# Performance work log

Measured on AMD Instinct MI355X. Metric: run time of the kernel, lower is better.

## Reference

```python
import jax, jax.numpy as jnp
import numpy as np

MARGIN = 1.0
EPS = 1e-05
B = 8192
D = 128
NUM_CLASSES = 256


def setup_inputs() -> dict:
    key = jax.random.key(0)
    k1, k2 = jax.random.split(key)
    feature = jax.random.normal(k1, (B, D), dtype=jnp.float32)
    label = jax.random.randint(k2, (B,), 0, NUM_CLASSES, dtype=jnp.int32)
    return {"feature": feature, "label": label}


def reference(feature, label):
    # Pairwise Euclidean distance matrix: ||x_i||^2 + ||x_j||^2 - 2 x_i.x_j + eps, then sqrt
    sq = jnp.sum(feature * feature, axis=1, keepdims=True)  # [B, 1]
    dist = jnp.sqrt(jnp.maximum(sq + sq.T - 2.0 * (feature @ feature.T) + EPS, 0.0))  # [B, B]

    same = label[:, None] == label[None, :]  # [B, B] bool, includes self on diagonal
    inf = jnp.array(jnp.inf, dtype=dist.dtype)

    # Original sorts each row and takes same[1]: the SECOND smallest same-label distance
    # (the smallest is the anchor itself, distance sqrt(eps)).
    d_same = jnp.where(same, dist, inf)
    two_smallest = -jax.lax.top_k(-d_same, 2)[0]  # [B, 2], ascending smallest two
    pos = two_smallest[:, 1]  # nearest positive excluding self

    # diff.min(): hardest (closest) negative per row
    neg = jnp.min(jnp.where(same, inf, dist), axis=1)

    hinge = jnp.maximum(MARGIN + pos - neg, 0.0)
    return jnp.mean(hinge)
```

## Files before the change

kernel.cpp:

```cpp
#include <hip/hip_runtime.h>
#include <math.h>


#define BN 8192
#define MARGIN_F 1.0f
#define EPS_F 1e-5f

typedef __attribute__((ext_vector_type(8))) short short8;
typedef __attribute__((ext_vector_type(4))) float floatx4;

__device__ __forceinline__ unsigned short bf16_rne(float x, float& r) {
    unsigned u = __float_as_uint(x);
    u += 0x7FFF + ((u >> 16) & 1);
    unsigned short h = (unsigned short)(u >> 16);
    r = __uint_as_float(((unsigned)h) << 16);
    return h;
}

__global__ __launch_bounds__(256) void prep_kernel(const float* __restrict__ f,
                                                   const int* __restrict__ lbl,
                                                   short8* __restrict__ fbT,
                                                   float2* __restrict__ lsq,
                                                   float* __restrict__ g_acc,
                                                   unsigned* __restrict__ counter) {
    int gid = blockIdx.x * 256 + threadIdx.x;
    if (gid == 0) { *g_acc = 0.f; *counter = 0u; }
    int row = gid >> 3, part = gid & 7;
    const float4* f4 = (const float4*)f + (size_t)row * 32 + part * 4;
    float s = 0.f;
#pragma unroll
    for (int cc = 0; cc < 2; ++cc) {
        float4 v0 = f4[cc * 2], v1 = f4[cc * 2 + 1];
        float r0, r1, r2, r3, r4, r5, r6, r7;
        short8 o;
        o[0] = (short)bf16_rne(v0.x, r0);
        o[1] = (short)bf16_rne(v0.y, r1);
        o[2] = (short)bf16_rne(v0.z, r2);
        o[3] = (short)bf16_rne(v0.w, r3);
        o[4] = (short)bf16_rne(v1.x, r4);
        o[5] = (short)bf16_rne(v1.y, r5);
        o[6] = (short)bf16_rne(v1.z, r6);
        o[7] = (short)bf16_rne(v1.w, r7);
        fbT[(size_t)(part * 2 + cc) * BN + row] = o;
        s += r0 * r0 + r1 * r1 + r2 * r2 + r3 * r3 +
             r4 * r4 + r5 * r5 + r6 * r6 + r7 * r7;
    }
    s += __shfl_xor(s, 1, 8);
    s += __shfl_xor(s, 2, 8);
    s += __shfl_xor(s, 4, 8);
    if (part == 0) {
        float2 p;
        p.x = s;
        p.y = __int_as_float(lbl[row]);
        lsq[row] = p;
    }
}

__device__ __forceinline__ void stage_tile(const short8* __restrict__ fbT,
                                           short8* tile, int j0, int wv, int lane) {
#pragma unroll
    for (int it = 0; it < 2; ++it) {
        int s = wv * 128 + it * 64;
        int kc = (s >> 5) + (lane >> 5);
        int col = lane & 31;
        const short8* g = fbT + ((size_t)kc * BN + j0 + col);
        __builtin_amdgcn_global_load_lds(
            (const __attribute__((address_space(1))) void*)g,
            (__attribute__((address_space(3))) void*)(tile + s),
            16, 0, 0);
    }
}

template <bool DIAG>
__device__ __forceinline__ void jt_loop(const short8* __restrict__ fbT,
                                        short8 (*Bt)[512],
                                        const float2* lsq_sh,
                                        const short8 a[2][4], const int li[2][4],
                                        float n1[2][4], float ss1[2][4],
                                        int wv, int lane, int c, int q,
                                        int i0, int jb) {
    for (int jt = 0; jt < 16; ++jt) {
        const short8* cur = Bt[jt & 1];
        if (jt < 15) stage_tile(fbT, Bt[1 - (jt & 1)], jb + (jt + 1) * 32, wv, lane);

        int ljv[2]; float sjv[2];
#pragma unroll
        for (int nf = 0; nf < 2; ++nf) {
            float2 p = lsq_sh[jt * 32 + nf * 16 + c];
            sjv[nf] = p.x;
            ljv[nf] = __float_as_int(p.y);
        }

        int dd = DIAG ? ((i0 + q * 4) - (jb + jt * 32 + c)) : 0;

        short8 b[4][2];
#pragma unroll
        for (int ks = 0; ks < 4; ++ks)
#pragma unroll
            for (int nf = 0; nf < 2; ++nf)
                b[ks][nf] = cur[(ks * 4 + q) * 32 + nf * 16 + c];

        floatx4 acc[2][2];
#pragma unroll
        for (int mf = 0; mf < 2; ++mf)
#pragma unroll
            for (int nf = 0; nf < 2; ++nf) acc[mf][nf] = (floatx4)0.f;

#pragma unroll
        for (int ks = 0; ks < 4; ++ks)
#pragma unroll
            for (int mf = 0; mf < 2; ++mf)
#pragma unroll
                for (int nf = 0; nf < 2; ++nf)
                    acc[mf][nf] = __builtin_amdgcn_mfma_f32_16x16x32_bf16(
                        a[mf][ks], b[ks][nf], acc[mf][nf], 0, 0, 0);

#pragma unroll
        for (int nf = 0; nf < 2; ++nf)
#pragma unroll
            for (int mf = 0; mf < 2; ++mf)
#pragma unroll
                for (int rg = 0; rg < 4; ++rg) {
                    float v = fmaf(-2.0f, acc[mf][nf][rg], sjv[nf]);
                    bool same = (li[mf][rg] == ljv[nf]);
                    float vd = same ? INFINITY : v;
                    n1[mf][rg] = fminf(n1[mf][rg], vd);
                    bool excl = same;
                    if (DIAG) excl = same && (dd != (nf * 16 - mf * 16 - rg));
                    float vs = excl ? v : INFINITY;
                    ss1[mf][rg] = fminf(ss1[mf][rg], vs);
                }
        __syncthreads();
    }
}

__global__ __launch_bounds__(256, 4) void work_kernel(const short8* __restrict__ fbT,
                                                      const float2* __restrict__ lsq,
                                                      float* __restrict__ part_n1,
                                                      float* __restrict__ part_p1) {
    const int t = threadIdx.x;
    const int lane = t & 63;
    const int wv = t >> 6;
    const int q = lane >> 4, c = lane & 15;
    const int bid = blockIdx.x;

    __shared__ short8 Bt[2][512];
    __shared__ float2 lsq_sh[512];

    const int ib = bid & 63;
    const int g = bid >> 6;
    const int i0 = ib * 128 + wv * 32;
    const int jb = g * 512;
    const bool diag = ((ib >> 2) == g);

    stage_tile(fbT, Bt[0], jb, wv, lane);

    lsq_sh[t] = lsq[jb + t];
    lsq_sh[t + 256] = lsq[jb + t + 256];

    short8 a[2][4];
#pragma unroll
    for (int mf = 0; mf < 2; ++mf) {
        int row = i0 + mf * 16 + c;
#pragma unroll
        for (int ks = 0; ks < 4; ++ks)
            a[mf][ks] = fbT[(size_t)(ks * 4 + q) * BN + row];
    }
    int li[2][4];
#pragma unroll
    for (int mf = 0; mf < 2; ++mf)
#pragma unroll
        for (int rg = 0; rg < 4; ++rg)
            li[mf][rg] = __float_as_int(lsq[i0 + mf * 16 + q * 4 + rg].y);

    float n1[2][4], ss1[2][4];
#pragma unroll
    for (int mf = 0; mf < 2; ++mf)
#pragma unroll
        for (int rg = 0; rg < 4; ++rg) {
            n1[mf][rg] = INFINITY;
            ss1[mf][rg] = INFINITY;
        }

    __syncthreads();

    if (diag)
        jt_loop<true>(fbT, Bt, lsq_sh, a, li, n1, ss1, wv, lane, c, q, i0, jb);
    else
        jt_loop<false>(fbT, Bt, lsq_sh, a, li, n1, ss1, wv, lane, c, q, i0, jb);

#pragma unroll
    for (int m = 1; m < 16; m <<= 1) {
#pragma unroll
        for (int mf = 0; mf < 2; ++mf)
#pragma unroll
            for (int rg = 0; rg < 4; ++rg) {
                n1[mf][rg] = fminf(n1[mf][rg], __shfl_xor(n1[mf][rg], m, 16));
                ss1[mf][rg] = fminf(ss1[mf][rg], __shfl_xor(ss1[mf][rg], m, 16));
            }
    }
    if (c == 0) {
#pragma unroll
        for (int mf = 0; mf < 2; ++mf)
#pragma unroll
            for (int rg = 0; rg < 4; ++rg) {
                int idx = g * BN + i0 + mf * 16 + q * 4 + rg;
                part_n1[idx] = n1[mf][rg];
                part_p1[idx] = ss1[mf][rg];
            }
    }
}

__global__ __launch_bounds__(128) void merge_kernel(const float* __restrict__ part_n1,
                                                    const float* __restrict__ part_p1,
                                                    const float2* __restrict__ lsq,
                                                    float* __restrict__ g_acc,
                                                    unsigned* __restrict__ counter,
                                                    float* __restrict__ out) {
    int r = blockIdx.x * 128 + threadIdx.x;
    float n = INFINITY, ss = INFINITY;
#pragma unroll
    for (int k = 0; k < 16; ++k) {
        n = fminf(n, part_n1[k * BN + r]);
        ss = fminf(ss, part_p1[k * BN + r]);
    }
    float si = lsq[r].x;
    float pos = sqrtf(fmaxf(si + ss + EPS_F, 0.f));
    float neg = sqrtf(fmaxf(si + n + EPS_F, 0.f));
    float h = fmaxf(MARGIN_F + pos - neg, 0.f);
    __shared__ float red[2];
#pragma unroll
    for (int m = 32; m >= 1; m >>= 1) h += __shfl_down(h, m, 64);
    if ((threadIdx.x & 63) == 0) red[threadIdx.x >> 6] = h;
    __syncthreads();
    if (threadIdx.x == 0) {
        atomicAdd(g_acc, red[0] + red[1]);
        __threadfence();
        unsigned old = atomicAdd(counter, 1u);
        if (old == 63u) {
            float tot = atomicAdd(g_acc, 0.0f);
            out[0] = tot / (float)BN;
        }
    }
}

extern "C" void kernel_launch(void* const* d_in, const int* in_sizes, int n_in,
                              void* d_out, int out_size, void* d_ws, size_t ws_size,
                              hipStream_t stream) {
    const float* f = (const float*)d_in[0];
    const int* lbl = (const int*)d_in[1];
    char* ws = (char*)d_ws;
    float2* lsq = (float2*)ws;
    short8* fbT = (short8*)(ws + 65536);
    float* part_n1 = (float*)(ws + 65536 + 2097152);
    float* part_p1 = (float*)(ws + 65536 + 2097152 + 524288);
    float* g_acc = (float*)(ws + 65536 + 2097152 + 1048576);
    unsigned* counter = (unsigned*)(g_acc + 1);
    float* out = (float*)d_out;

    prep_kernel<<<256, 256, 0, stream>>>(f, lbl, fbT, lsq, g_acc, counter);
    work_kernel<<<1024, 256, 0, stream>>>(fbT, lsq, part_n1, part_p1);
    merge_kernel<<<64, 128, 0, stream>>>(part_n1, part_p1, lsq, g_acc, counter, out);
}
```

Before: 85.24 us.

## Sort rows by label to skip same-label epilogue work on most tiles

Adds a histogram/prefix-sum kernel and scatters rows into label-sorted order during prep. The work kernel can then compute, per block, the column range holding any label present in its row block. Only tiles in that range run the full same-label/positive epilogue; all other tiles do a plain negative min. This removes compare and select work from most tiles, at the cost of an extra launch, atomic-based scatter (which makes row order nondeterministic), and scattered writes. The merge kernel must handle the permuted order, and it is not shown.

```diff
diff --git a/kernel.cpp b/kernel.cpp
--- a/kernel.cpp
+++ b/kernel.cpp
@@ -17,15 +17,52 @@
     return h;
 }
 
+__global__ __launch_bounds__(256) void hist_kernel(const int* __restrict__ lbl,
+                                                   int* __restrict__ base,
+                                                   int* __restrict__ cursor,
+                                                   float* __restrict__ g_acc,
+                                                   unsigned* __restrict__ counter) {
+    __shared__ int h[256];
+    __shared__ int sc[257];
+    const int t = threadIdx.x;
+    if (t == 0) { *g_acc = 0.f; *counter = 0u; }
+    h[t] = 0;
+    __syncthreads();
+    const int4* l4 = (const int4*)lbl;
+    for (int i = t; i < BN / 4; i += 256) {
+        int4 L = l4[i];
+        atomicAdd(&h[L.x], 1);
+        atomicAdd(&h[L.y], 1);
+        atomicAdd(&h[L.z], 1);
+        atomicAdd(&h[L.w], 1);
+    }
+    __syncthreads();
+    if (t == 0) sc[0] = 0;
+    sc[t + 1] = h[t];
+    __syncthreads();
+    for (int off = 1; off < 256; off <<= 1) {
+        int add = (t >= off) ? sc[t + 1 - off] : 0;
+        __syncthreads();
+        sc[t + 1] += add;
+        __syncthreads();
+    }
+    base[t] = sc[t];
+    cursor[t] = sc[t];
+    if (t == 255) base[256] = sc[256];
+}
+
 __global__ __launch_bounds__(256) void prep_kernel(const float* __restrict__ f,
                                                    const int* __restrict__ lbl,
+                                                   int* __restrict__ cursor,
                                                    short8* __restrict__ fbT,
-                                                   float2* __restrict__ lsq,
-                                                   float* __restrict__ g_acc,
-                                                   unsigned* __restrict__ counter) {
+                                                   float2* __restrict__ lsq) {
     int gid = blockIdx.x * 256 + threadIdx.x;
-    if (gid == 0) { *g_acc = 0.f; *counter = 0u; }
     int row = gid >> 3, part = gid & 7;
+    int lb = lbl[row];
+    int dst = 0;
+    if (part == 0) dst = atomicAdd(&cursor[lb], 1);
+    dst = __shfl(dst, 0, 8);
+
     const float4* f4 = (const float4*)f + (size_t)row * 32 + part * 4;
     float s = 0.f;
 #pragma unroll
@@ -41,7 +78,7 @@
         o[5] = (short)bf16_rne(v1.y, r5);
         o[6] = (short)bf16_rne(v1.z, r6);
         o[7] = (short)bf16_rne(v1.w, r7);
-        fbT[(size_t)(part * 2 + cc) * BN + row] = o;
+        fbT[(size_t)(part * 2 + cc) * BN + dst] = o;
         s += r0 * r0 + r1 * r1 + r2 * r2 + r3 * r3 +
              r4 * r4 + r5 * r5 + r6 * r6 + r7 * r7;
     }
@@ -51,8 +88,8 @@
     if (part == 0) {
         float2 p;
         p.x = s;
-        p.y = __int_as_float(lbl[row]);
-        lsq[row] = p;
+        p.y = __int_as_float(lb);
+        lsq[dst] = p;
     }
 }
 
@@ -71,71 +108,9 @@
     }
 }
 
-template <bool DIAG>
-__device__ __forceinline__ void jt_loop(const short8* __restrict__ fbT,
-                                        short8 (*Bt)[512],
-                                        const float2* lsq_sh,
-                                        const short8 a[2][4], const int li[2][4],
-                                        float n1[2][4], float ss1[2][4],
-                                        int wv, int lane, int c, int q,
-                                        int i0, int jb) {
-    for (int jt = 0; jt < 16; ++jt) {
-        const short8* cur = Bt[jt & 1];
-        if (jt < 15) stage_tile(fbT, Bt[1 - (jt & 1)], jb + (jt + 1) * 32, wv, lane);
-
-        int ljv[2]; float sjv[2];
-#pragma unroll
-        for (int nf = 0; nf < 2; ++nf) {
-            float2 p = lsq_sh[jt * 32 + nf * 16 + c];
-            sjv[nf] = p.x;
-            ljv[nf] = __float_as_int(p.y);
-        }
-
-        int dd = DIAG ? ((i0 + q * 4) - (jb + jt * 32 + c)) : 0;
-
-        short8 b[4][2];
-#pragma unroll
-        for (int ks = 0; ks < 4; ++ks)
-#pragma unroll
-            for (int nf = 0; nf < 2; ++nf)
-                b[ks][nf] = cur[(ks * 4 + q) * 32 + nf * 16 + c];
-
-        floatx4 acc[2][2];
-#pragma unroll
-        for (int mf = 0; mf < 2; ++mf)
-#pragma unroll
-            for (int nf = 0; nf < 2; ++nf) acc[mf][nf] = (floatx4)0.f;
-
-#pragma unroll
-        for (int ks = 0; ks < 4; ++ks)
-#pragma unroll
-            for (int mf = 0; mf < 2; ++mf)
-#pragma unroll
-                for (int nf = 0; nf < 2; ++nf)
-                    acc[mf][nf] = __builtin_amdgcn_mfma_f32_16x16x32_bf16(
-                        a[mf][ks], b[ks][nf], acc[mf][nf], 0, 0, 0);
-
-#pragma unroll
-        for (int nf = 0; nf < 2; ++nf)
-#pragma unroll
-            for (int mf = 0; mf < 2; ++mf)
-#pragma unroll
-                for (int rg = 0; rg < 4; ++rg) {
-                    float v = fmaf(-2.0f, acc[mf][nf][rg], sjv[nf]);
-                    bool same = (li[mf][rg] == ljv[nf]);
-                    float vd = same ? INFINITY : v;
-                    n1[mf][rg] = fminf(n1[mf][rg], vd);
-                    bool excl = same;
-                    if (DIAG) excl = same && (dd != (nf * 16 - mf * 16 - rg));
-                    float vs = excl ? v : INFINITY;
-                    ss1[mf][rg] = fminf(ss1[mf][rg], vs);
-                }
-        __syncthreads();
-    }
-}
-
 __global__ __launch_bounds__(256, 4) void work_kernel(const short8* __restrict__ fbT,
                                                       const float2* __restrict__ lsq,
+                                                      const int* __restrict__ base,
                                                       float* __restrict__ part_n1,
                                                       float* __restrict__ part_p1) {
     const int t = threadIdx.x;
@@ -151,12 +126,22 @@
     const int g = bid >> 6;
     const int i0 = ib * 128 + wv * 32;
     const int jb = g * 512;
-    const bool diag = ((ib >> 2) == g);
 
     stage_tile(fbT, Bt[0], jb, wv, lane);
 
     lsq_sh[t] = lsq[jb + t];
     lsq_sh[t + 256] = lsq[jb + t + 256];
+
+    const int ibase = ib * 128;
+    const int cLo = __float_as_int(lsq[ibase].y);
+    const int cHi = __float_as_int(lsq[ibase + 127].y);
+    const int jLoCol = base[cLo];
+    const int jHiCol = base[cHi + 1];
+    const int mLo = jLoCol > jb ? jLoCol : jb;
+    const int mHi = jHiCol < jb + 512 ? jHiCol : jb + 512;
+    const bool blkmask = mLo < mHi;
+    const int jtLo = blkmask ? (mLo - jb) >> 5 : 16;
+    const int jtHi = blkmask ? (mHi - 1 - jb) >> 5 : -1;
 
     short8 a[2][4];
 #pragma unroll
@@ -184,10 +169,71 @@
 
     __syncthreads();
 
-    if (diag)
-        jt_loop<true>(fbT, Bt, lsq_sh, a, li, n1, ss1, wv, lane, c, q, i0, jb);
-    else
-        jt_loop<false>(fbT, Bt, lsq_sh, a, li, n1, ss1, wv, lane, c, q, i0, jb);
+    for (int jt = 0; jt < 16; ++jt) {
+        const short8* cur = Bt[jt & 1];
+        if (jt < 15) stage_tile(fbT, Bt[1 - (jt & 1)], jb + (jt + 1) * 32, wv, lane);
+
+        float sjv[2]; int ljv[2];
+#pragma unroll
+        for (int nf = 0; nf < 2; ++nf) {
+            float2 p = lsq_sh[jt * 32 + nf * 16 + c];
+            sjv[nf] = p.x;
+            ljv[nf] = __float_as_int(p.y);
+        }
+
+        short8 b[4][2];
+#pragma unroll
+        for (int ks = 0; ks < 4; ++ks)
+#pragma unroll
+            for (int nf = 0; nf < 2; ++nf)
+                b[ks][nf] = cur[(ks * 4 + q) * 32 + nf * 16 + c];
+
+        floatx4 acc[2][2];
+#pragma unroll
+        for (int mf = 0; mf < 2; ++mf)
+#pragma unroll
+            for (int nf = 0; nf < 2; ++nf) acc[mf][nf] = (floatx4)0.f;
+
+#pragma unroll
+        for (int ks = 0; ks < 4; ++ks)
+#pragma unroll
+            for (int mf = 0; mf < 2; ++mf)
+#pragma unroll
+                for (int nf = 0; nf < 2; ++nf)
+                    acc[mf][nf] = __builtin_amdgcn_mfma_f32_16x16x32_bf16(
+                        a[mf][ks], b[ks][nf], acc[mf][nf], 0, 0, 0);
+
+        if (jt >= jtLo && jt <= jtHi) {
+            int dd = (i0 + q * 4) - (jb + jt * 32 + c);
+#pragma unroll
+            for (int mf = 0; mf < 2; ++mf)
+#pragma unroll
+                for (int rg = 0; rg < 4; ++rg) {
+                    float v0 = fmaf(-2.0f, acc[mf][0][rg], sjv[0]);
+                    float v1 = fmaf(-2.0f, acc[mf][1][rg], sjv[1]);
+                    bool sm0 = (li[mf][rg] == ljv[0]);
+                    bool sm1 = (li[mf][rg] == ljv[1]);
+                    float vd0 = sm0 ? INFINITY : v0;
+                    float vd1 = sm1 ? INFINITY : v1;
+                    n1[mf][rg] = fminf(fminf(n1[mf][rg], vd0), vd1);
+                    bool ex0 = sm0 && (dd != (0 * 16 - mf * 16 - rg));
+                    bool ex1 = sm1 && (dd != (1 * 16 - mf * 16 - rg));
+                    float vs0 = ex0 ? v0 : INFINITY;
+                    float vs1 = ex1 ? v1 : INFINITY;
+                    ss1[mf][rg] = fminf(fminf(ss1[mf][rg], vs0), vs1);
+                }
+        } else {
+#pragma unroll
+            for (int mf = 0; mf < 2; ++mf)
+#pragma unroll
+                for (int rg = 0; rg < 4; ++rg) {
+                    float v0 = fmaf(-2.0f, acc[mf][0][rg], sjv[0]);
+                    float v1 = fmaf(-2.0f, acc[mf][1][rg], sjv[1]);
+                    n1[mf][rg] = fminf(fminf(n1[mf][rg], v0), v1);
+                }
+        }
+        __syncthreads();
+    }
 
 #pragma unroll
     for (int m = 1; m < 16; m <<= 1) {
@@ -254,11 +300,15 @@
     short8* fbT = (short8*)(ws + 65536);
     float* part_n1 = (float*)(ws + 65536 + 2097152);
     float* part_p1 = (float*)(ws + 65536 + 2097152 + 524288);
-    float* g_acc = (float*)(ws + 65536 + 2097152 + 1048576);
-    unsigned* counter = (unsigned*)(g_acc + 1);
+    char* tail = ws + 65536 + 2097152 + 1048576;
+    float* g_acc = (float*)tail;
+    unsigned* counter = (unsigned*)(tail + 4);
+    int* base = (int*)(tail + 64);
+    int* cursor = (int*)(tail + 2112);
     float* out = (float*)d_out;
 
-    prep_kernel<<<256, 256, 0, stream>>>(f, lbl, fbT, lsq, g_acc, counter);
-    work_kernel<<<1024, 256, 0, stream>>>(fbT, lsq, part_n1, part_p1);
+    hist_kernel<<<1, 256, 0, stream>>>(lbl, base, cursor, g_acc, counter);
+    prep_kernel<<<256, 256, 0, stream>>>(f, lbl, cursor, fbT, lsq);
+    work_kernel<<<1024, 256, 0, stream>>>(fbT, lsq, base, part_n1, part_p1);
     merge_kernel<<<64, 128, 0, stream>>>(part_n1, part_p1, lsq, g_acc, counter, out);
 }
```

After: 95.79 us. 12.4% more time.
